# Kernel optimization log

Measured on AMD Instinct MI355X. Metric: run time of the kernel, lower is better.

## Reference

```python
import jax, jax.numpy as jnp
import numpy as np

B, S, D = 2, 2048, 768
HD = 64          # hardcoded head_dim in module
NH = D // HD     # 12 query heads
NKV = max(1, NH // 3)  # 4 kv heads
GROUPS = NH // NKV     # 3
WINDOW = 384
THETA = 10000.0
EPS = 1e-6


def setup_inputs() -> dict:
    key = jax.random.key(0)
    ks = jax.random.split(key, 5)
    return {
        "hidden_states": jax.random.normal(ks[0], (B, S, D), dtype=jnp.float32),
        "q_w": jax.random.normal(ks[1], (NH * HD, D), dtype=jnp.float32) * 0.02,
        "k_w": jax.random.normal(ks[2], (NKV * HD, D), dtype=jnp.float32) * 0.02,
        "v_w": jax.random.normal(ks[3], (NKV * HD, D), dtype=jnp.float32) * 0.02,
        "o_w": jax.random.normal(ks[4], (D, NH * HD), dtype=jnp.float32) * 0.02,
        "q_ln_w": jnp.ones((HD,), dtype=jnp.float32),
        "k_ln_w": jnp.ones((HD,), dtype=jnp.float32),
    }


def _rmsnorm(x, w):
    var = jnp.mean(jnp.square(x.astype(jnp.float32)), axis=-1, keepdims=True)
    return w * (x * jax.lax.rsqrt(var + EPS)).astype(x.dtype)


def _rotate_half(x):
    x1, x2 = jnp.split(x, 2, axis=-1)
    return jnp.concatenate((-x2, x1), axis=-1)


def _rope_cos_sin(seq_len, dtype):
    inv_freq = 1.0 / (THETA ** (jnp.arange(0, HD, 2, dtype=jnp.float32) / HD))
    t = jnp.arange(seq_len, dtype=jnp.float32)
    freqs = jnp.outer(t, inv_freq)            # [S, HD/2]
    emb = jnp.concatenate((freqs, freqs), -1)  # [S, HD]
    return jnp.cos(emb).astype(dtype), jnp.sin(emb).astype(dtype)


def reference(hidden_states, q_w, k_w, v_w, o_w, q_ln_w, k_ln_w):
    b, s, _ = hidden_states.shape
    # projections (nn.Linear: y = x @ W.T)
    q = hidden_states @ q_w.T   # [B,S,NH*HD]
    k = hidden_states @ k_w.T   # [B,S,NKV*HD]
    v = hidden_states @ v_w.T

    q = _rmsnorm(q.reshape(b, s, NH, HD), q_ln_w).transpose(0, 2, 1, 3)      # [B,NH,S,HD]
    k = _rmsnorm(k.reshape(b, s, NKV, HD), k_ln_w).transpose(0, 2, 1, 3)     # [B,NKV,S,HD]
    v = v.reshape(b, s, NKV, HD).transpose(0, 2, 1, 3)                       # [B,NKV,S,HD]

    cos, sin = _rope_cos_sin(s, q.dtype)  # [S,HD]
    cos = cos[None, None]
    sin = sin[None, None]
    q = q * cos + _rotate_half(q) * sin
    k = k * cos + _rotate_half(k) * sin

    # grouped-query repeat: [B,NKV,S,HD] -> [B,NH,S,HD]
    k = jnp.repeat(k, GROUPS, axis=1)
    v = jnp.repeat(v, GROUPS, axis=1)

    scores = jnp.einsum("bhqd,bhkd->bhqk", q, k) / np.sqrt(HD)
    # causal + sliding-window mask: allow i-WINDOW < j <= i
    idx = jnp.arange(s)
    rel = idx[None, :] - idx[:, None]  # j - i
    allowed = (rel <= 0) & (rel > -WINDOW)
    scores = jnp.where(allowed[None, None], scores, -jnp.inf)

    attn = jax.nn.softmax(scores.astype(jnp.float32), axis=-1).astype(q.dtype)
    out = jnp.einsum("bhqk,bhkd->bhqd", attn, v)       # [B,NH,S,HD]
    out = out.transpose(0, 2, 1, 3).reshape(b, s, NH * HD)
    return out @ o_w.T
```

## Files before the change

kernel.cpp:

```cpp
#include <hip/hip_runtime.h>
#include <hip/hip_bf16.h>

typedef __hip_bfloat16 bf16;
typedef __attribute__((ext_vector_type(8))) short bf16x8;
typedef __attribute__((ext_vector_type(4))) float f32x4;

#define MFMA16(a, b, c) __builtin_amdgcn_mfma_f32_16x16x32_bf16((a), (b), (c), 0, 0, 0)


__device__ __forceinline__ void st4bf(bf16* p, float4 v) {
    bf16 t[4];
    t[0] = __float2bfloat16(v.x); t[1] = __float2bfloat16(v.y);
    t[2] = __float2bfloat16(v.z); t[3] = __float2bfloat16(v.w);
    *reinterpret_cast<uint2*>(p) = *reinterpret_cast<const uint2*>(t);
}

__global__ __launch_bounds__(256) void k_prep(
    const float* __restrict__ hs, const float* __restrict__ qw,
    const float* __restrict__ kw, const float* __restrict__ vw,
    const float* __restrict__ ow,
    bf16* __restrict__ hsb, bf16* __restrict__ qwb, bf16* __restrict__ kwb,
    bf16* __restrict__ vwb, bf16* __restrict__ owb, float2* __restrict__ tab)
{
    const int bid = blockIdx.x, tid = threadIdx.x;
    const float* src; bf16* dst; int rel;
    if (bid < 3072)      { src = hs; dst = hsb; rel = bid; }
    else if (bid < 3648) { src = qw; dst = qwb; rel = bid - 3072; }
    else if (bid < 3840) { src = kw; dst = kwb; rel = bid - 3648; }
    else if (bid < 4032) { src = vw; dst = vwb; rel = bid - 3840; }
    else if (bid < 4608) { src = ow; dst = owb; rel = bid - 4032; }
    else {
        int i = (bid - 4608) * 256 + tid;
        int f = i & 31;
        float ang = (float)(i >> 5) * expf(-(float)f * 0.28782313662425572f);
        float sn, cs; sincosf(ang, &sn, &cs);
        tab[i] = make_float2(cs, sn);
        return;
    }
    int i = (rel * 256 + tid) * 4;
    float4 v = *reinterpret_cast<const float4*>(src + i);
    st4bf(dst + i, v);
}

__global__ __launch_bounds__(256) void k_qkv(
    const bf16* __restrict__ hsb, const bf16* __restrict__ qwb,
    const bf16* __restrict__ kwb, const bf16* __restrict__ vwb,
    const float* __restrict__ qln, const float* __restrict__ kln,
    const float2* __restrict__ tab,
    bf16* __restrict__ qo, bf16* __restrict__ ko, bf16* __restrict__ vto)
{
    __shared__ bf16 As[2][64 * 72];
    __shared__ bf16 Bs[2][64 * 72];
    const int tid = threadIdx.x;
    const int w = tid >> 6, l = tid & 63;
    const int lm = l & 15, lg = l >> 4;
    const int m0 = blockIdx.x * 64;
    const int nblk = blockIdx.y;

    const bf16* wsrc; int wrow0, kind, head;
    if (nblk < 12)      { wsrc = qwb; wrow0 = nblk * 64;        kind = 0; head = nblk; }
    else if (nblk < 16) { wsrc = kwb; wrow0 = (nblk - 12) * 64; kind = 1; head = nblk - 12; }
    else                { wsrc = vwb; wrow0 = (nblk - 16) * 64; kind = 2; head = nblk - 16; }

    const int sr = tid >> 2, sc = (tid & 3) * 16;
    const bf16* aptr = hsb  + (size_t)(m0 + sr) * 768 + sc;
    const bf16* bptr = wsrc + (size_t)(wrow0 + sr) * 768 + sc;

    bf16x8 ra0 = *(const bf16x8*)(aptr);
    bf16x8 ra1 = *(const bf16x8*)(aptr + 8);
    bf16x8 rb0 = *(const bf16x8*)(bptr);
    bf16x8 rb1 = *(const bf16x8*)(bptr + 8);

    f32x4 acc[4] = {};
    for (int t = 0; t < 12; ++t) {
        const int p = t & 1;
        *(bf16x8*)(&As[p][sr * 72 + sc])     = ra0;
        *(bf16x8*)(&As[p][sr * 72 + sc + 8]) = ra1;
        *(bf16x8*)(&Bs[p][sr * 72 + sc])     = rb0;
        *(bf16x8*)(&Bs[p][sr * 72 + sc + 8]) = rb1;
        __syncthreads();
        if (t < 11) {
            const int off = (t + 1) * 64;
            ra0 = *(const bf16x8*)(aptr + off);
            ra1 = *(const bf16x8*)(aptr + off + 8);
            rb0 = *(const bf16x8*)(bptr + off);
            rb1 = *(const bf16x8*)(bptr + off + 8);
        }
        #pragma unroll
        for (int kk = 0; kk < 2; ++kk) {
            bf16x8 af = *(const bf16x8*)(&As[p][(w * 16 + lm) * 72 + kk * 32 + lg * 8]);
            #pragma unroll
            for (int ct = 0; ct < 4; ++ct) {
                bf16x8 bfr = *(const bf16x8*)(&Bs[p][(ct * 16 + lm) * 72 + kk * 32 + lg * 8]);
                acc[ct] = MFMA16(af, bfr, acc[ct]);
            }
        }
    }

    const int b  = m0 >> 11;
    const int s0 = m0 & 2047;

    if (kind == 2) {
        bf16* base = vto + (size_t)(b * 4 + head) * 64 * 2048;
        #pragma unroll
        for (int r = 0; r < 4; ++r) {
            const int s = s0 + w * 16 + lg * 4 + r;
            #pragma unroll
            for (int ct = 0; ct < 4; ++ct)
                base[(size_t)(ct * 16 + lm) * 2048 + s] = __float2bfloat16(acc[ct][r]);
        }
        return;
    }

    const float* ln = (kind == 0) ? qln : kln;
    float lw[4];
    #pragma unroll
    for (int ct = 0; ct < 4; ++ct) lw[ct] = ln[ct * 16 + lm];

    bf16* base = (kind == 0) ? qo + ((size_t)(b * 12 + head) * 2048 + s0) * 64
                             : ko + ((size_t)(b * 4  + head) * 2048 + s0) * 64;
    #pragma unroll
    for (int r = 0; r < 4; ++r) {
        float n0 = acc[0][r], n1 = acc[1][r], n2 = acc[2][r], n3 = acc[3][r];
        float ss = n0 * n0 + n1 * n1 + n2 * n2 + n3 * n3;
        ss += __shfl_xor(ss, 1);
        ss += __shfl_xor(ss, 2);
        ss += __shfl_xor(ss, 4);
        ss += __shfl_xor(ss, 8);
        float rms = rsqrtf(ss * (1.0f / 64.0f) + 1e-6f);
        n0 *= rms * lw[0]; n1 *= rms * lw[1]; n2 *= rms * lw[2]; n3 *= rms * lw[3];
        const int row = w * 16 + lg * 4 + r;
        const float2* tp = tab + (size_t)(s0 + row) * 32;
        float2 t0 = tp[lm], t1 = tp[lm + 16];
        bf16* dst = base + (size_t)row * 64;
        dst[lm]      = __float2bfloat16(n0 * t0.x - n2 * t0.y);
        dst[lm + 16] = __float2bfloat16(n1 * t1.x - n3 * t1.y);
        dst[lm + 32] = __float2bfloat16(n2 * t0.x + n0 * t0.y);
        dst[lm + 48] = __float2bfloat16(n3 * t1.x + n1 * t1.y);
    }
}

__global__ __launch_bounds__(256) void k_attn(
    const bf16* __restrict__ qi, const bf16* __restrict__ ki,
    const bf16* __restrict__ vti, bf16* __restrict__ ao)
{
    __shared__ bf16 Ks[2][64 * 72];
    __shared__ bf16 Vs[2][64 * 72];
    __shared__ bf16 Ps[64 * 72];
    const int tid = threadIdx.x;
    const int w = tid >> 6, l = tid & 63;
    const int lm = l & 15, lg = l >> 4;
    const int qb = blockIdx.x, h = blockIdx.y, b = blockIdx.z;
    const int kv = h / 3;
    const int q0 = qb * 64;
    const float SCL2 = 0.18033688011117042f;

    const bf16* qbase = qi + ((size_t)((b * 12 + h) * 2048 + q0 + w * 16 + lm)) * 64 + lg * 8;
    bf16x8 qf0 = *(const bf16x8*)(qbase);
    bf16x8 qf1 = *(const bf16x8*)(qbase + 32);

    f32x4 oacc[4] = {};
    float m_[4], l_[4];
    #pragma unroll
    for (int r = 0; r < 4; ++r) { m_[r] = -INFINITY; l_[r] = 0.f; }

    const int sr = tid >> 2, sc = (tid & 3) * 16;
    const bf16* kgb = ki  + (size_t)(b * 4 + kv) * 2048 * 64;
    const bf16* vgb = vti + (size_t)(b * 4 + kv) * 64 * 2048;

    const int kb_lo = (qb > 6) ? (qb - 6) : 0;
    bf16x8 rk0, rk1, rv0, rv1;
    {
        const bf16* kp = kgb + (size_t)(kb_lo * 64 + sr) * 64 + sc;
        const bf16* vp = vgb + (size_t)sr * 2048 + kb_lo * 64 + sc;
        rk0 = *(const bf16x8*)(kp);
        rk1 = *(const bf16x8*)(kp + 8);
        rv0 = *(const bf16x8*)(vp);
        rv1 = *(const bf16x8*)(vp + 8);
    }

    for (int kb = kb_lo; kb <= qb; ++kb) {
        const int p = (kb - kb_lo) & 1;
        const int k0 = kb * 64;

        *(bf16x8*)(&Ks[p][sr * 72 + sc])     = rk0;
        *(bf16x8*)(&Ks[p][sr * 72 + sc + 8]) = rk1;
        *(bf16x8*)(&Vs[p][sr * 72 + sc])     = rv0;
        *(bf16x8*)(&Vs[p][sr * 72 + sc + 8]) = rv1;
        __syncthreads();
        if (kb < qb) {
            const bf16* kp = kgb + (size_t)(k0 + 64 + sr) * 64 + sc;
            const bf16* vp = vgb + (size_t)sr * 2048 + k0 + 64 + sc;
            rk0 = *(const bf16x8*)(kp);
            rk1 = *(const bf16x8*)(kp + 8);
            rv0 = *(const bf16x8*)(vp);
            rv1 = *(const bf16x8*)(vp + 8);
        }

        f32x4 sacc[4];
        #pragma unroll
        for (int kt = 0; kt < 4; ++kt) {
            bf16x8 kf0 = *(const bf16x8*)(&Ks[p][(kt * 16 + lm) * 72 + lg * 8]);
            bf16x8 kf1 = *(const bf16x8*)(&Ks[p][(kt * 16 + lm) * 72 + 32 + lg * 8]);
            f32x4 z = {0.f, 0.f, 0.f, 0.f};
            z = MFMA16(qf0, kf0, z);
            sacc[kt] = MFMA16(qf1, kf1, z);
        }

        float pmax[4] = {-INFINITY, -INFINITY, -INFINITY, -INFINITY};
        const bool need_mask = (kb == qb) || (kb == qb - 6);
        if (need_mask) {
            #pragma unroll
            for (int kt = 0; kt < 4; ++kt)
                #pragma unroll
                for (int r = 0; r < 4; ++r) {
                    int kgl = k0 + kt * 16 + lm;
                    int qgl = q0 + w * 16 + lg * 4 + r;
                    bool ok = (kgl <= qgl) && (kgl > qgl - 384);
                    float s = ok ? sacc[kt][r] * SCL2 : -INFINITY;
                    sacc[kt][r] = s;
                    pmax[r] = fmaxf(pmax[r], s);
                }
        } else {
            #pragma unroll
            for (int kt = 0; kt < 4; ++kt)
                #pragma unroll
                for (int r = 0; r < 4; ++r) {
                    float s = sacc[kt][r] * SCL2;
                    sacc[kt][r] = s;
                    pmax[r] = fmaxf(pmax[r], s);
                }
        }
        #pragma unroll
        for (int r = 0; r < 4; ++r) {
            float t = pmax[r];
            t = fmaxf(t, __shfl_xor(t, 1));
            t = fmaxf(t, __shfl_xor(t, 2));
            t = fmaxf(t, __shfl_xor(t, 4));
            t = fmaxf(t, __shfl_xor(t, 8));
            pmax[r] = t;
        }

        if (need_mask) {
            #pragma unroll
            for (int r = 0; r < 4; ++r) {
                float mnew = fmaxf(m_[r], pmax[r]);
                float scale, rs = 0.f, pv[4];
                if (mnew > -INFINITY) {
                    scale = exp2f(m_[r] - mnew);
                    #pragma unroll
                    for (int kt = 0; kt < 4; ++kt) { pv[kt] = exp2f(sacc[kt][r] - mnew); rs += pv[kt]; }
                } else {
                    scale = 1.f;
                    #pragma unroll
                    for (int kt = 0; kt < 4; ++kt) pv[kt] = 0.f;
                }
                m_[r] = mnew;
                rs += __shfl_xor(rs, 1);
                rs += __shfl_xor(rs, 2);
                rs += __shfl_xor(rs, 4);
                rs += __shfl_xor(rs, 8);
                l_[r] = l_[r] * scale + rs;
                #pragma unroll
                for (int dt = 0; dt < 4; ++dt) oacc[dt][r] *= scale;
                #pragma unroll
                for (int kt = 0; kt < 4; ++kt)
                    Ps[(w * 16 + lg * 4 + r) * 72 + kt * 16 + lm] = __float2bfloat16(pv[kt]);
            }
        } else {
            #pragma unroll
            for (int r = 0; r < 4; ++r) {
                float mnew = fmaxf(m_[r], pmax[r]);
                float scale = exp2f(m_[r] - mnew);
                float rs = 0.f, pv[4];
                #pragma unroll
                for (int kt = 0; kt < 4; ++kt) { pv[kt] = exp2f(sacc[kt][r] - mnew); rs += pv[kt]; }
                m_[r] = mnew;
                rs += __shfl_xor(rs, 1);
                rs += __shfl_xor(rs, 2);
                rs += __shfl_xor(rs, 4);
                rs += __shfl_xor(rs, 8);
                l_[r] = l_[r] * scale + rs;
                #pragma unroll
                for (int dt = 0; dt < 4; ++dt) oacc[dt][r] *= scale;
                #pragma unroll
                for (int kt = 0; kt < 4; ++kt)
                    Ps[(w * 16 + lg * 4 + r) * 72 + kt * 16 + lm] = __float2bfloat16(pv[kt]);
            }
        }

        bf16x8 pf0 = *(const bf16x8*)(&Ps[(w * 16 + lm) * 72 + lg * 8]);
        bf16x8 pf1 = *(const bf16x8*)(&Ps[(w * 16 + lm) * 72 + 32 + lg * 8]);
        #pragma unroll
        for (int dt = 0; dt < 4; ++dt) {
            bf16x8 vf0 = *(const bf16x8*)(&Vs[p][(dt * 16 + lm) * 72 + lg * 8]);
            bf16x8 vf1 = *(const bf16x8*)(&Vs[p][(dt * 16 + lm) * 72 + 32 + lg * 8]);
            oacc[dt] = MFMA16(pf0, vf0, oacc[dt]);
            oacc[dt] = MFMA16(pf1, vf1, oacc[dt]);
        }
    }

    #pragma unroll
    for (int r = 0; r < 4; ++r) {
        float inv = 1.f / l_[r];
        bf16* dst = ao + ((size_t)(b * 2048 + q0 + w * 16 + lg * 4 + r)) * 768 + h * 64;
        #pragma unroll
        for (int dt = 0; dt < 4; ++dt)
            dst[dt * 16 + lm] = __float2bfloat16(oacc[dt][r] * inv);
    }
}

__global__ __launch_bounds__(256) void k_oproj(
    const bf16* __restrict__ A, const bf16* __restrict__ W, float* __restrict__ out)
{
    __shared__ bf16 As[2][64 * 72];
    __shared__ bf16 Bs[2][64 * 72];
    const int tid = threadIdx.x;
    const int w = tid >> 6, l = tid & 63;
    const int lm = l & 15, lg = l >> 4;
    const int m0 = blockIdx.x * 64, n0 = blockIdx.y * 64;

    const int sr = tid >> 2, sc = (tid & 3) * 16;
    const bf16* aptr = A + (size_t)(m0 + sr) * 768 + sc;
    const bf16* bptr = W + (size_t)(n0 + sr) * 768 + sc;

    bf16x8 ra0 = *(const bf16x8*)(aptr);
    bf16x8 ra1 = *(const bf16x8*)(aptr + 8);
    bf16x8 rb0 = *(const bf16x8*)(bptr);
    bf16x8 rb1 = *(const bf16x8*)(bptr + 8);

    f32x4 acc[4] = {};
    for (int t = 0; t < 12; ++t) {
        const int p = t & 1;
        *(bf16x8*)(&As[p][sr * 72 + sc])     = ra0;
        *(bf16x8*)(&As[p][sr * 72 + sc + 8]) = ra1;
        *(bf16x8*)(&Bs[p][sr * 72 + sc])     = rb0;
        *(bf16x8*)(&Bs[p][sr * 72 + sc + 8]) = rb1;
        __syncthreads();
        if (t < 11) {
            const int off = (t + 1) * 64;
            ra0 = *(const bf16x8*)(aptr + off);
            ra1 = *(const bf16x8*)(aptr + off + 8);
            rb0 = *(const bf16x8*)(bptr + off);
            rb1 = *(const bf16x8*)(bptr + off + 8);
        }
        #pragma unroll
        for (int kk = 0; kk < 2; ++kk) {
            bf16x8 af = *(const bf16x8*)(&As[p][(w * 16 + lm) * 72 + kk * 32 + lg * 8]);
            #pragma unroll
            for (int ct = 0; ct < 4; ++ct) {
                bf16x8 bfr = *(const bf16x8*)(&Bs[p][(ct * 16 + lm) * 72 + kk * 32 + lg * 8]);
                acc[ct] = MFMA16(af, bfr, acc[ct]);
            }
        }
    }

    #pragma unroll
    for (int r = 0; r < 4; ++r) {
        float* dst = out + (size_t)(m0 + w * 16 + lg * 4 + r) * 768 + n0;
        #pragma unroll
        for (int ct = 0; ct < 4; ++ct)
            dst[ct * 16 + lm] = acc[ct][r];
    }
}

extern "C" void kernel_launch(void* const* d_in, const int* in_sizes, int n_in,
                              void* d_out, int out_size, void* d_ws, size_t ws_size,
                              hipStream_t stream) {
    const float* hs  = (const float*)d_in[0];
    const float* qw  = (const float*)d_in[1];
    const float* kw  = (const float*)d_in[2];
    const float* vw  = (const float*)d_in[3];
    const float* ow  = (const float*)d_in[4];
    const float* qln = (const float*)d_in[5];
    const float* kln = (const float*)d_in[6];
    float* out = (float*)d_out;

    float2* tab  = (float2*)d_ws;
    bf16*   q_ws = (bf16*)(tab + 65536);
    bf16*   k_ws = q_ws + 3145728;
    bf16*   vt_ws= k_ws + 1048576;
    bf16*   x_ws = vt_ws + 1048576;
    bf16*   qwb  = x_ws + 3145728;
    bf16*   kwb  = qwb + 589824;
    bf16*   vwb  = kwb + 196608;
    bf16*   owb  = vwb + 196608;

    k_prep<<<dim3(4864), 256, 0, stream>>>(hs, qw, kw, vw, ow, x_ws, qwb, kwb, vwb, owb, tab);
    k_qkv<<<dim3(64, 20, 1), 256, 0, stream>>>(x_ws, qwb, kwb, vwb, qln, kln, tab, q_ws, k_ws, vt_ws);
    k_attn<<<dim3(32, 12, 2), 256, 0, stream>>>(q_ws, k_ws, vt_ws, x_ws);
    k_oproj<<<dim3(64, 12, 1), 256, 0, stream>>>(x_ws, owb, out);
}
```

Before: 69.49 us.

## Process all three GQA query heads per attention block to share K/V tiles

```diff
diff --git a/kernel.cpp b/kernel.cpp
--- a/kernel.cpp
+++ b/kernel.cpp
@@ -150,23 +150,28 @@
     const int tid = threadIdx.x;
     const int w = tid >> 6, l = tid & 63;
     const int lm = l & 15, lg = l >> 4;
-    const int qb = blockIdx.x, h = blockIdx.y, b = blockIdx.z;
-    const int kv = h / 3;
+    const int qb = blockIdx.x, kvh = blockIdx.y, b = blockIdx.z;
     const int q0 = qb * 64;
     const float SCL2 = 0.18033688011117042f;
 
-    const bf16* qbase = qi + ((size_t)((b * 12 + h) * 2048 + q0 + w * 16 + lm)) * 64 + lg * 8;
-    bf16x8 qf0 = *(const bf16x8*)(qbase);
-    bf16x8 qf1 = *(const bf16x8*)(qbase + 32);
-
-    f32x4 oacc[4] = {};
-    float m_[4], l_[4];
-    #pragma unroll
-    for (int r = 0; r < 4; ++r) { m_[r] = -INFINITY; l_[r] = 0.f; }
+    bf16x8 qf0[3], qf1[3];
+    #pragma unroll
+    for (int hh = 0; hh < 3; ++hh) {
+        const bf16* qbase = qi + ((size_t)((b * 12 + kvh * 3 + hh) * 2048 + q0 + w * 16 + lm)) * 64 + lg * 8;
+        qf0[hh] = *(const bf16x8*)(qbase);
+        qf1[hh] = *(const bf16x8*)(qbase + 32);
+    }
+
+    f32x4 oacc[3][4] = {};
+    float m_[3][4], l_[3][4];
+    #pragma unroll
+    for (int hh = 0; hh < 3; ++hh)
+        #pragma unroll
+        for (int r = 0; r < 4; ++r) { m_[hh][r] = -INFINITY; l_[hh][r] = 0.f; }
 
     const int sr = tid >> 2, sc = (tid & 3) * 16;
-    const bf16* kgb = ki  + (size_t)(b * 4 + kv) * 2048 * 64;
-    const bf16* vgb = vti + (size_t)(b * 4 + kv) * 64 * 2048;
+    const bf16* kgb = ki  + (size_t)(b * 4 + kvh) * 2048 * 64;
+    const bf16* vgb = vti + (size_t)(b * 4 + kvh) * 64 * 2048;
 
     const int kb_lo = (qb > 6) ? (qb - 6) : 0;
     bf16x8 rk0, rk1, rv0, rv1;
@@ -197,117 +202,129 @@
             rv1 = *(const bf16x8*)(vp + 8);
         }
 
-        f32x4 sacc[4];
+        f32x4 sacc[3][4];
         #pragma unroll
         for (int kt = 0; kt < 4; ++kt) {
             bf16x8 kf0 = *(const bf16x8*)(&Ks[p][(kt * 16 + lm) * 72 + lg * 8]);
             bf16x8 kf1 = *(const bf16x8*)(&Ks[p][(kt * 16 + lm) * 72 + 32 + lg * 8]);
-            f32x4 z = {0.f, 0.f, 0.f, 0.f};
-            z = MFMA16(qf0, kf0, z);
-            sacc[kt] = MFMA16(qf1, kf1, z);
-        }
-
-        float pmax[4] = {-INFINITY, -INFINITY, -INFINITY, -INFINITY};
+            #pragma unroll
+            for (int hh = 0; hh < 3; ++hh) {
+                f32x4 z = {0.f, 0.f, 0.f, 0.f};
+                z = MFMA16(qf0[hh], kf0, z);
+                sacc[hh][kt] = MFMA16(qf1[hh], kf1, z);
+            }
+        }
+
         const bool need_mask = (kb == qb) || (kb == qb - 6);
-        if (need_mask) {
-            #pragma unroll
-            for (int kt = 0; kt < 4; ++kt)
+        bf16x8 pf0[3], pf1[3];
+        #pragma unroll
+        for (int hh = 0; hh < 3; ++hh) {
+            float pmax[4] = {-INFINITY, -INFINITY, -INFINITY, -INFINITY};
+            if (need_mask) {
+                #pragma unroll
+                for (int kt = 0; kt < 4; ++kt)
+                    #pragma unroll
+                    for (int r = 0; r < 4; ++r) {
+                        int kgl = k0 + kt * 16 + lm;
+                        int qgl = q0 + w * 16 + lg * 4 + r;
+                        bool ok = (kgl <= qgl) && (kgl > qgl - 384);
+                        float s = ok ? sacc[hh][kt][r] * SCL2 : -INFINITY;
+                        sacc[hh][kt][r] = s;
+                        pmax[r] = fmaxf(pmax[r], s);
+                    }
+            } else {
+                #pragma unroll
+                for (int kt = 0; kt < 4; ++kt)
+                    #pragma unroll
+                    for (int r = 0; r < 4; ++r) {
+                        float s = sacc[hh][kt][r] * SCL2;
+                        sacc[hh][kt][r] = s;
+                        pmax[r] = fmaxf(pmax[r], s);
+                    }
+            }
+            #pragma unroll
+            for (int r = 0; r < 4; ++r) {
+                float t = pmax[r];
+                t = fmaxf(t, __shfl_xor(t, 1));
+                t = fmaxf(t, __shfl_xor(t, 2));
+                t = fmaxf(t, __shfl_xor(t, 4));
+                t = fmaxf(t, __shfl_xor(t, 8));
+                pmax[r] = t;
+            }
+
+            if (need_mask) {
                 #pragma unroll
                 for (int r = 0; r < 4; ++r) {
-                    int kgl = k0 + kt * 16 + lm;
-                    int qgl = q0 + w * 16 + lg * 4 + r;
-                    bool ok = (kgl <= qgl) && (kgl > qgl - 384);
-                    float s = ok ? sacc[kt][r] * SCL2 : -INFINITY;
-                    sacc[kt][r] = s;
-                    pmax[r] = fmaxf(pmax[r], s);
+                    float mnew = fmaxf(m_[hh][r], pmax[r]);
+                    float scale, rs = 0.f, pv[4];
+                    if (mnew > -INFINITY) {
+                        scale = exp2f(m_[hh][r] - mnew);
+                        #pragma unroll
+                        for (int kt = 0; kt < 4; ++kt) { pv[kt] = exp2f(sacc[hh][kt][r] - mnew); rs += pv[kt]; }
+                    } else {
+                        scale = 1.f;
+                        #pragma unroll
+                        for (int kt = 0; kt < 4; ++kt) pv[kt] = 0.f;
+                    }
+                    m_[hh][r] = mnew;
+                    rs += __shfl_xor(rs, 1);
+                    rs += __shfl_xor(rs, 2);
+                    rs += __shfl_xor(rs, 4);
+                    rs += __shfl_xor(rs, 8);
+                    l_[hh][r] = l_[hh][r] * scale + rs;
+                    #pragma unroll
+                    for (int dt = 0; dt < 4; ++dt) oacc[hh][dt][r] *= scale;
+                    #pragma unroll
+                    for (int kt = 0; kt < 4; ++kt)
+                        Ps[(w * 16 + lg * 4 + r) * 72 + kt * 16 + lm] = __float2bfloat16(pv[kt]);
                 }
-        } else {
-            #pragma unroll
-            for (int kt = 0; kt < 4; ++kt)
+            } else {
                 #pragma unroll
                 for (int r = 0; r < 4; ++r) {
-                    float s = sacc[kt][r] * SCL2;
-                    sacc[kt][r] = s;
-                    pmax[r] = fmaxf(pmax[r], s);
+                    float mnew = fmaxf(m_[hh][r], pmax[r]);
+                    float scale = exp2f(m_[hh][r] - mnew);
+                    float rs = 0.f, pv[4];
+                    #pragma unroll
+                    for (int kt = 0; kt < 4; ++kt) { pv[kt] = exp2f(sacc[hh][kt][r] - mnew); rs += pv[kt]; }
+                    m_[hh][r] = mnew;
+                    rs += __shfl_xor(rs, 1);
+                    rs += __shfl_xor(rs, 2);
+                    rs += __shfl_xor(rs, 4);
+                    rs += __shfl_xor(rs, 8);
+                    l_[hh][r] = l_[hh][r] * scale + rs;
+                    #pragma unroll
+                    for (int dt = 0; dt < 4; ++dt) oacc[hh][dt][r] *= scale;
+                    #pragma unroll
+                    for (int kt = 0; kt < 4; ++kt)
+                        Ps[(w * 16 + lg * 4 + r) * 72 + kt * 16 + lm] = __float2bfloat16(pv[kt]);
                 }
-        }
-        #pragma unroll
-        for (int r = 0; r < 4; ++r) {
-            float t = pmax[r];
-            t = fmaxf(t, __shfl_xor(t, 1));
-            t = fmaxf(t, __shfl_xor(t, 2));
-            t = fmaxf(t, __shfl_xor(t, 4));
-            t = fmaxf(t, __shfl_xor(t, 8));
-            pmax[r] = t;
-        }
-
-        if (need_mask) {
-            #pragma unroll
-            for (int r = 0; r < 4; ++r) {
-                float mnew = fmaxf(m_[r], pmax[r]);
-                float scale, rs = 0.f, pv[4];
-                if (mnew > -INFINITY) {
-                    scale = exp2f(m_[r] - mnew);
-                    #pragma unroll
-                    for (int kt = 0; kt < 4; ++kt) { pv[kt] = exp2f(sacc[kt][r] - mnew); rs += pv[kt]; }
-                } else {
-                    scale = 1.f;
-                    #pragma unroll
-                    for (int kt = 0; kt < 4; ++kt) pv[kt] = 0.f;
-                }
-                m_[r] = mnew;
-                rs += __shfl_xor(rs, 1);
-                rs += __shfl_xor(rs, 2);
-                rs += __shfl_xor(rs, 4);
-                rs += __shfl_xor(rs, 8);
-                l_[r] = l_[r] * scale + rs;
-                #pragma unroll
-                for (int dt = 0; dt < 4; ++dt) oacc[dt][r] *= scale;
-                #pragma unroll
-                for (int kt = 0; kt < 4; ++kt)
-                    Ps[(w * 16 + lg * 4 + r) * 72 + kt * 16 + lm] = __float2bfloat16(pv[kt]);
-            }
-        } else {
-            #pragma unroll
-            for (int r = 0; r < 4; ++r) {
-                float mnew = fmaxf(m_[r], pmax[r]);
-                float scale = exp2f(m_[r] - mnew);
-                float rs = 0.f, pv[4];
-                #pragma unroll
-                for (int kt = 0; kt < 4; ++kt) { pv[kt] = exp2f(sacc[kt][r] - mnew); rs += pv[kt]; }
-                m_[r] = mnew;
-                rs += __shfl_xor(rs, 1);
-                rs += __shfl_xor(rs, 2);
-                rs += __shfl_xor(rs, 4);
-                rs += __shfl_xor(rs, 8);
-                l_[r] = l_[r] * scale + rs;
-                #pragma unroll
-                for (int dt = 0; dt < 4; ++dt) oacc[dt][r] *= scale;
-                #pragma unroll
-                for (int kt = 0; kt < 4; ++kt)
-                    Ps[(w * 16 + lg * 4 + r) * 72 + kt * 16 + lm] = __float2bfloat16(pv[kt]);
-            }
-        }
-
-        bf16x8 pf0 = *(const bf16x8*)(&Ps[(w * 16 + lm) * 72 + lg * 8]);
-        bf16x8 pf1 = *(const bf16x8*)(&Ps[(w * 16 + lm) * 72 + 32 + lg * 8]);
+            }
+            pf0[hh] = *(const bf16x8*)(&Ps[(w * 16 + lm) * 72 + lg * 8]);
+            pf1[hh] = *(const bf16x8*)(&Ps[(w * 16 + lm) * 72 + 32 + lg * 8]);
+        }
+
         #pragma unroll
         for (int dt = 0; dt < 4; ++dt) {
             bf16x8 vf0 = *(const bf16x8*)(&Vs[p][(dt * 16 + lm) * 72 + lg * 8]);
             bf16x8 vf1 = *(const bf16x8*)(&Vs[p][(dt * 16 + lm) * 72 + 32 + lg * 8]);
-            oacc[dt] = MFMA16(pf0, vf0, oacc[dt]);
-            oacc[dt] = MFMA16(pf1, vf1, oacc[dt]);
-        }
-    }
-
-    #pragma unroll
-    for (int r = 0; r < 4; ++r) {
-        float inv = 1.f / l_[r];
-        bf16* dst = ao + ((size_t)(b * 2048 + q0 + w * 16 + lg * 4 + r)) * 768 + h * 64;
-        #pragma unroll
-        for (int dt = 0; dt < 4; ++dt)
-            dst[dt * 16 + lm] = __float2bfloat16(oacc[dt][r] * inv);
-    }
+            #pragma unroll
+            for (int hh = 0; hh < 3; ++hh) {
+                oacc[hh][dt] = MFMA16(pf0[hh], vf0, oacc[hh][dt]);
+                oacc[hh][dt] = MFMA16(pf1[hh], vf1, oacc[hh][dt]);
+            }
+        }
+    }
+
+    #pragma unroll
+    for (int hh = 0; hh < 3; ++hh)
+        #pragma unroll
+        for (int r = 0; r < 4; ++r) {
+            float inv = 1.f / l_[hh][r];
+            bf16* dst = ao + ((size_t)(b * 2048 + q0 + w * 16 + lg * 4 + r)) * 768 + (kvh * 3 + hh) * 64;
+            #pragma unroll
+            for (int dt = 0; dt < 4; ++dt)
+                dst[dt * 16 + lm] = __float2bfloat16(oacc[hh][dt][r] * inv);
+        }
 }
 
 __global__ __launch_bounds__(256) void k_oproj(
@@ -388,6 +405,6 @@
 
     k_prep<<<dim3(4864), 256, 0, stream>>>(hs, qw, kw, vw, ow, x_ws, qwb, kwb, vwb, owb, tab);
     k_qkv<<<dim3(64, 20, 1), 256, 0, stream>>>(x_ws, qwb, kwb, vwb, qln, kln, tab, q_ws, k_ws, vt_ws);
-    k_attn<<<dim3(32, 12, 2), 256, 0, stream>>>(q_ws, k_ws, vt_ws, x_ws);
+    k_attn<<<dim3(32, 4, 2), 256, 0, stream>>>(q_ws, k_ws, vt_ws, x_ws);
     k_oproj<<<dim3(64, 12, 1), 256, 0, stream>>>(x_ws, owb, out);
 }
```

Result: slower. 79.46 us (+14.4%).

## Rewrite attention with 32x32 MFMA, register-resident P, and prescaled Q

Applied to the files above, without the earlier changes.

```diff
diff --git a/kernel.cpp b/kernel.cpp
--- a/kernel.cpp
+++ b/kernel.cpp
@@ -4,8 +4,10 @@
 typedef __hip_bfloat16 bf16;
 typedef __attribute__((ext_vector_type(8))) short bf16x8;
 typedef __attribute__((ext_vector_type(4))) float f32x4;
+typedef __attribute__((ext_vector_type(16))) float f32x16;
 
 #define MFMA16(a, b, c) __builtin_amdgcn_mfma_f32_16x16x32_bf16((a), (b), (c), 0, 0, 0)
+#define MFMA32(a, b, c) __builtin_amdgcn_mfma_f32_32x32x16_bf16((a), (b), (c), 0, 0, 0)
 
 
 __device__ __forceinline__ void st4bf(bf16* p, float4 v) {
@@ -113,9 +115,10 @@
     }
 
     const float* ln = (kind == 0) ? qln : kln;
+    const float qscl = (kind == 0) ? 0.18033688011117042f : 1.0f;
     float lw[4];
     #pragma unroll
-    for (int ct = 0; ct < 4; ++ct) lw[ct] = ln[ct * 16 + lm];
+    for (int ct = 0; ct < 4; ++ct) lw[ct] = ln[ct * 16 + lm] * qscl;
 
     bf16* base = (kind == 0) ? qo + ((size_t)(b * 12 + head) * 2048 + s0) * 64
                              : ko + ((size_t)(b * 4  + head) * 2048 + s0) * 64;
@@ -140,173 +143,171 @@
     }
 }
 
-__global__ __launch_bounds__(256) void k_attn(
+__global__ __launch_bounds__(128) void k_attn(
     const bf16* __restrict__ qi, const bf16* __restrict__ ki,
     const bf16* __restrict__ vti, bf16* __restrict__ ao)
 {
     __shared__ bf16 Ks[2][64 * 72];
     __shared__ bf16 Vs[2][64 * 72];
-    __shared__ bf16 Ps[64 * 72];
     const int tid = threadIdx.x;
     const int w = tid >> 6, l = tid & 63;
-    const int lm = l & 15, lg = l >> 4;
+    const int p = l >> 5, c31 = l & 31;
     const int qb = blockIdx.x, h = blockIdx.y, b = blockIdx.z;
     const int kv = h / 3;
     const int q0 = qb * 64;
-    const float SCL2 = 0.18033688011117042f;
-
-    const bf16* qbase = qi + ((size_t)((b * 12 + h) * 2048 + q0 + w * 16 + lm)) * 64 + lg * 8;
-    bf16x8 qf0 = *(const bf16x8*)(qbase);
-    bf16x8 qf1 = *(const bf16x8*)(qbase + 32);
-
-    f32x4 oacc[4] = {};
-    float m_[4], l_[4];
-    #pragma unroll
-    for (int r = 0; r < 4; ++r) { m_[r] = -INFINITY; l_[r] = 0.f; }
-
-    const int sr = tid >> 2, sc = (tid & 3) * 16;
+    const int qw0 = q0 + w * 32;
+    const int q_g = qw0 + c31;
+
+    const bf16* qrow = qi + ((size_t)((b * 12 + h) * 2048 + q_g)) * 64 + p * 8;
+    bf16x8 qf0 = *(const bf16x8*)(qrow);
+    bf16x8 qf1 = *(const bf16x8*)(qrow + 16);
+    bf16x8 qf2 = *(const bf16x8*)(qrow + 32);
+    bf16x8 qf3 = *(const bf16x8*)(qrow + 48);
+
+    f32x16 oacc0 = {}, oacc1 = {};
+    float m_ = -INFINITY, l_ = 0.f;
+
+    const int sr = tid >> 1, sc = (tid & 1) * 32;
     const bf16* kgb = ki  + (size_t)(b * 4 + kv) * 2048 * 64;
     const bf16* vgb = vti + (size_t)(b * 4 + kv) * 64 * 2048;
 
     const int kb_lo = (qb > 6) ? (qb - 6) : 0;
-    bf16x8 rk0, rk1, rv0, rv1;
+    bf16x8 rk[4], rv[4];
     {
         const bf16* kp = kgb + (size_t)(kb_lo * 64 + sr) * 64 + sc;
         const bf16* vp = vgb + (size_t)sr * 2048 + kb_lo * 64 + sc;
-        rk0 = *(const bf16x8*)(kp);
-        rk1 = *(const bf16x8*)(kp + 8);
-        rv0 = *(const bf16x8*)(vp);
-        rv1 = *(const bf16x8*)(vp + 8);
+        #pragma unroll
+        for (int j = 0; j < 4; ++j) {
+            rk[j] = *(const bf16x8*)(kp + j * 8);
+            rv[j] = *(const bf16x8*)(vp + j * 8);
+        }
     }
 
     for (int kb = kb_lo; kb <= qb; ++kb) {
-        const int p = (kb - kb_lo) & 1;
+        const int pb = (kb - kb_lo) & 1;
         const int k0 = kb * 64;
 
-        *(bf16x8*)(&Ks[p][sr * 72 + sc])     = rk0;
-        *(bf16x8*)(&Ks[p][sr * 72 + sc + 8]) = rk1;
-        *(bf16x8*)(&Vs[p][sr * 72 + sc])     = rv0;
-        *(bf16x8*)(&Vs[p][sr * 72 + sc + 8]) = rv1;
+        #pragma unroll
+        for (int j = 0; j < 4; ++j) {
+            *(bf16x8*)(&Ks[pb][sr * 72 + sc + j * 8]) = rk[j];
+            *(bf16x8*)(&Vs[pb][sr * 72 + sc + j * 8]) = rv[j];
+        }
         __syncthreads();
         if (kb < qb) {
             const bf16* kp = kgb + (size_t)(k0 + 64 + sr) * 64 + sc;
             const bf16* vp = vgb + (size_t)sr * 2048 + k0 + 64 + sc;
-            rk0 = *(const bf16x8*)(kp);
-            rk1 = *(const bf16x8*)(kp + 8);
-            rv0 = *(const bf16x8*)(vp);
-            rv1 = *(const bf16x8*)(vp + 8);
-        }
-
-        f32x4 sacc[4];
-        #pragma unroll
-        for (int kt = 0; kt < 4; ++kt) {
-            bf16x8 kf0 = *(const bf16x8*)(&Ks[p][(kt * 16 + lm) * 72 + lg * 8]);
-            bf16x8 kf1 = *(const bf16x8*)(&Ks[p][(kt * 16 + lm) * 72 + 32 + lg * 8]);
-            f32x4 z = {0.f, 0.f, 0.f, 0.f};
-            z = MFMA16(qf0, kf0, z);
-            sacc[kt] = MFMA16(qf1, kf1, z);
-        }
-
-        float pmax[4] = {-INFINITY, -INFINITY, -INFINITY, -INFINITY};
-        const bool need_mask = (kb == qb) || (kb == qb - 6);
+            #pragma unroll
+            for (int j = 0; j < 4; ++j) {
+                rk[j] = *(const bf16x8*)(kp + j * 8);
+                rv[j] = *(const bf16x8*)(vp + j * 8);
+            }
+        }
+
+        f32x16 s0 = {}, s1 = {};
+        {
+            const bf16* kbase = &Ks[pb][c31 * 72 + p * 8];
+            s0 = MFMA32(*(const bf16x8*)(kbase),      qf0, s0);
+            s0 = MFMA32(*(const bf16x8*)(kbase + 16), qf1, s0);
+            s0 = MFMA32(*(const bf16x8*)(kbase + 32), qf2, s0);
+            s0 = MFMA32(*(const bf16x8*)(kbase + 48), qf3, s0);
+            const bf16* kbase1 = kbase + 32 * 72;
+            s1 = MFMA32(*(const bf16x8*)(kbase1),      qf0, s1);
+            s1 = MFMA32(*(const bf16x8*)(kbase1 + 16), qf1, s1);
+            s1 = MFMA32(*(const bf16x8*)(kbase1 + 32), qf2, s1);
+            s1 = MFMA32(*(const bf16x8*)(kbase1 + 48), qf3, s1);
+        }
+
+        const bool need_mask = (64 * kb + 63 > qw0) || (64 * kb <= qw0 - 353);
         if (need_mask) {
             #pragma unroll
-            for (int kt = 0; kt < 4; ++kt)
-                #pragma unroll
-                for (int r = 0; r < 4; ++r) {
-                    int kgl = k0 + kt * 16 + lm;
-                    int qgl = q0 + w * 16 + lg * 4 + r;
-                    bool ok = (kgl <= qgl) && (kgl > qgl - 384);
-                    float s = ok ? sacc[kt][r] * SCL2 : -INFINITY;
-                    sacc[kt][r] = s;
-                    pmax[r] = fmaxf(pmax[r], s);
-                }
+            for (int r = 0; r < 16; ++r) {
+                int kl = (r & 3) + 8 * (r >> 2) + 4 * p;
+                int kg0 = k0 + kl, kg1 = k0 + 32 + kl;
+                bool ok0 = (kg0 <= q_g) && (kg0 > q_g - 384);
+                bool ok1 = (kg1 <= q_g) && (kg1 > q_g - 384);
+                s0[r] = ok0 ? s0[r] : -INFINITY;
+                s1[r] = ok1 ? s1[r] : -INFINITY;
+            }
+        }
+
+        float tmax = s0[0];
+        #pragma unroll
+        for (int r = 1; r < 16; ++r) tmax = fmaxf(tmax, s0[r]);
+        #pragma unroll
+        for (int r = 0; r < 16; ++r) tmax = fmaxf(tmax, s1[r]);
+        tmax = fmaxf(tmax, __shfl_xor(tmax, 32));
+
+        float mnew = fmaxf(m_, tmax);
+        float scale, rs = 0.f;
+        if (mnew > -INFINITY) {
+            scale = exp2f(m_ - mnew);
+            #pragma unroll
+            for (int r = 0; r < 16; ++r) { s0[r] = exp2f(s0[r] - mnew); rs += s0[r]; }
+            #pragma unroll
+            for (int r = 0; r < 16; ++r) { s1[r] = exp2f(s1[r] - mnew); rs += s1[r]; }
         } else {
-            #pragma unroll
-            for (int kt = 0; kt < 4; ++kt)
-                #pragma unroll
-                for (int r = 0; r < 4; ++r) {
-                    float s = sacc[kt][r] * SCL2;
-                    sacc[kt][r] = s;
-                    pmax[r] = fmaxf(pmax[r], s);
-                }
-        }
-        #pragma unroll
-        for (int r = 0; r < 4; ++r) {
-            float t = pmax[r];
-            t = fmaxf(t, __shfl_xor(t, 1));
-            t = fmaxf(t, __shfl_xor(t, 2));
-            t = fmaxf(t, __shfl_xor(t, 4));
-            t = fmaxf(t, __shfl_xor(t, 8));
-            pmax[r] = t;
-        }
-
-        if (need_mask) {
-            #pragma unroll
-            for (int r = 0; r < 4; ++r) {
-                float mnew = fmaxf(m_[r], pmax[r]);
-                float scale, rs = 0.f, pv[4];
-                if (mnew > -INFINITY) {
-                    scale = exp2f(m_[r] - mnew);
-                    #pragma unroll
-                    for (int kt = 0; kt < 4; ++kt) { pv[kt] = exp2f(sacc[kt][r] - mnew); rs += pv[kt]; }
-                } else {
-                    scale = 1.f;
-                    #pragma unroll
-                    for (int kt = 0; kt < 4; ++kt) pv[kt] = 0.f;
-                }
-                m_[r] = mnew;
-                rs += __shfl_xor(rs, 1);
-                rs += __shfl_xor(rs, 2);
-                rs += __shfl_xor(rs, 4);
-                rs += __shfl_xor(rs, 8);
-                l_[r] = l_[r] * scale + rs;
-                #pragma unroll
-                for (int dt = 0; dt < 4; ++dt) oacc[dt][r] *= scale;
-                #pragma unroll
-                for (int kt = 0; kt < 4; ++kt)
-                    Ps[(w * 16 + lg * 4 + r) * 72 + kt * 16 + lm] = __float2bfloat16(pv[kt]);
-            }
-        } else {
-            #pragma unroll
-            for (int r = 0; r < 4; ++r) {
-                float mnew = fmaxf(m_[r], pmax[r]);
-                float scale = exp2f(m_[r] - mnew);
-                float rs = 0.f, pv[4];
-                #pragma unroll
-                for (int kt = 0; kt < 4; ++kt) { pv[kt] = exp2f(sacc[kt][r] - mnew); rs += pv[kt]; }
-                m_[r] = mnew;
-                rs += __shfl_xor(rs, 1);
-                rs += __shfl_xor(rs, 2);
-                rs += __shfl_xor(rs, 4);
-                rs += __shfl_xor(rs, 8);
-                l_[r] = l_[r] * scale + rs;
-                #pragma unroll
-                for (int dt = 0; dt < 4; ++dt) oacc[dt][r] *= scale;
-                #pragma unroll
-                for (int kt = 0; kt < 4; ++kt)
-                    Ps[(w * 16 + lg * 4 + r) * 72 + kt * 16 + lm] = __float2bfloat16(pv[kt]);
-            }
-        }
-
-        bf16x8 pf0 = *(const bf16x8*)(&Ps[(w * 16 + lm) * 72 + lg * 8]);
-        bf16x8 pf1 = *(const bf16x8*)(&Ps[(w * 16 + lm) * 72 + 32 + lg * 8]);
-        #pragma unroll
-        for (int dt = 0; dt < 4; ++dt) {
-            bf16x8 vf0 = *(const bf16x8*)(&Vs[p][(dt * 16 + lm) * 72 + lg * 8]);
-            bf16x8 vf1 = *(const bf16x8*)(&Vs[p][(dt * 16 + lm) * 72 + 32 + lg * 8]);
-            oacc[dt] = MFMA16(pf0, vf0, oacc[dt]);
-            oacc[dt] = MFMA16(pf1, vf1, oacc[dt]);
-        }
-    }
-
+            scale = 1.f;
+            #pragma unroll
+            for (int r = 0; r < 16; ++r) { s0[r] = 0.f; s1[r] = 0.f; }
+        }
+        m_ = mnew;
+        rs += __shfl_xor(rs, 32);
+        l_ = l_ * scale + rs;
+        #pragma unroll
+        for (int r = 0; r < 16; ++r) { oacc0[r] *= scale; oacc1[r] *= scale; }
+
+        bf16x8 paf[4];
+        #pragma unroll
+        for (int kt = 0; kt < 2; ++kt) {
+            unsigned pk[8];
+            #pragma unroll
+            for (int i = 0; i < 8; ++i) {
+                float lo = (kt == 0) ? s0[2 * i] : s1[2 * i];
+                float hi = (kt == 0) ? s0[2 * i + 1] : s1[2 * i + 1];
+                bf16 blo = __float2bfloat16(lo), bhi = __float2bfloat16(hi);
+                pk[i] = ((unsigned)*(unsigned short*)&bhi << 16) | (unsigned)*(unsigned short*)&blo;
+            }
+            unsigned x[8];
+            #pragma unroll
+            for (int i = 0; i < 8; ++i) x[i] = (unsigned)__shfl_xor((int)pk[i], 32);
+            #pragma unroll
+            for (int s = 0; s < 2; ++s) {
+                union { int4 i4; bf16x8 v; } u;
+                u.i4.x = p ? (int)x[4 * s + 2] : (int)pk[4 * s];
+                u.i4.y = p ? (int)x[4 * s + 3] : (int)pk[4 * s + 1];
+                u.i4.z = p ? (int)pk[4 * s + 2] : (int)x[4 * s];
+                u.i4.w = p ? (int)pk[4 * s + 3] : (int)x[4 * s + 1];
+                paf[kt * 2 + s] = u.v;
+            }
+        }
+
+        {
+            const bf16* vbase = &Vs[pb][c31 * 72 + p * 8];
+            oacc0 = MFMA32(*(const bf16x8*)(vbase),      paf[0], oacc0);
+            oacc0 = MFMA32(*(const bf16x8*)(vbase + 16), paf[1], oacc0);
+            oacc0 = MFMA32(*(const bf16x8*)(vbase + 32), paf[2], oacc0);
+            oacc0 = MFMA32(*(const bf16x8*)(vbase + 48), paf[3], oacc0);
+            const bf16* vbase1 = vbase + 32 * 72;
+            oacc1 = MFMA32(*(const bf16x8*)(vbase1),      paf[0], oacc1);
+            oacc1 = MFMA32(*(const bf16x8*)(vbase1 + 16), paf[1], oacc1);
+            oacc1 = MFMA32(*(const bf16x8*)(vbase1 + 32), paf[2], oacc1);
+            oacc1 = MFMA32(*(const bf16x8*)(vbase1 + 48), paf[3], oacc1);
+        }
+        __syncthreads();
+    }
+
+    const float inv = 1.f / l_;
+    bf16* dst = ao + ((size_t)(b * 2048 + q_g)) * 768 + h * 64;
     #pragma unroll
-    for (int r = 0; r < 4; ++r) {
-        float inv = 1.f / l_[r];
-        bf16* dst = ao + ((size_t)(b * 2048 + q0 + w * 16 + lg * 4 + r)) * 768 + h * 64;
-        #pragma unroll
-        for (int dt = 0; dt < 4; ++dt)
-            dst[dt * 16 + lm] = __float2bfloat16(oacc[dt][r] * inv);
+    for (int g = 0; g < 4; ++g) {
+        union { uint2 u2; bf16 t[4]; } o0, o1;
+        #pragma unroll
+        for (int e = 0; e < 4; ++e) {
+            o0.t[e] = __float2bfloat16(oacc0[4 * g + e] * inv);
+            o1.t[e] = __float2bfloat16(oacc1[4 * g + e] * inv);
+        }
+        *reinterpret_cast<uint2*>(dst + 8 * g + 4 * p)      = o0.u2;
+        *reinterpret_cast<uint2*>(dst + 32 + 8 * g + 4 * p) = o1.u2;
     }
 }
 
@@ -388,6 +389,6 @@
 
     k_prep<<<dim3(4864), 256, 0, stream>>>(hs, qw, kw, vw, ow, x_ws, qwb, kwb, vwb, owb, tab);
     k_qkv<<<dim3(64, 20, 1), 256, 0, stream>>>(x_ws, qwb, kwb, vwb, qln, kln, tab, q_ws, k_ws, vt_ws);
-    k_attn<<<dim3(32, 12, 2), 256, 0, stream>>>(q_ws, k_ws, vt_ws, x_ws);
+    k_attn<<<dim3(32, 12, 2), 128, 0, stream>>>(q_ws, k_ws, vt_ws, x_ws);
     k_oproj<<<dim3(64, 12, 1), 256, 0, stream>>>(x_ws, owb, out);
 }
```

Result: no change. 68.22 us (-1.8%).
